# Kernel optimization log

Hardware: AMD Instinct MI355X
Metric: run time of the kernel (lower is better)

Reference implementation:

```python
import jax, jax.numpy as jnp
import numpy as np

B, T, D_MODEL, H, D = 2, 2048, 2048, 16, 128


def _rope_tables(t, d_half, base=10000.0):
    inv_freq = 1.0 / (base ** (jnp.arange(d_half, dtype=jnp.float32) / d_half))
    ang = jnp.arange(t, dtype=jnp.float32)[:, None] * inv_freq[None, :]  # (T, D/2)
    return jnp.cos(ang), jnp.sin(ang)


def setup_inputs() -> dict:
    key = jax.random.key(0)
    ks = jax.random.split(key, 5)
    x = jax.random.normal(ks[0], (B, T, D_MODEL), dtype=jnp.float32)
    mask = jnp.tril(jnp.ones((T, T), dtype=bool))  # causal boolean mask
    cos, sin = _rope_tables(T, D // 2)
    std = 1.0 / np.sqrt(D_MODEL)
    Wq = jax.random.normal(ks[1], (D_MODEL, H * D), dtype=jnp.float32) * std
    Wk = jax.random.normal(ks[2], (D_MODEL, H * D), dtype=jnp.float32) * std
    Wv = jax.random.normal(ks[3], (D_MODEL, H * D), dtype=jnp.float32) * std
    Wo = jax.random.normal(ks[4], (H * D, D_MODEL), dtype=jnp.float32) * std
    return {"x": x, "mask": mask, "cos": cos, "sin": sin,
            "Wq": Wq, "Wk": Wk, "Wv": Wv, "Wo": Wo}


def _apply_rope(x, cos, sin):
    # x: (B, H, T, D); cos/sin: (T, D/2)
    half = x.shape[-1] // 2
    x1, x2 = x[..., :half], x[..., half:]
    c = cos[None, None]
    s = sin[None, None]
    return jnp.concatenate([x1 * c - x2 * s, x1 * s + x2 * c], axis=-1)


def reference(x, mask, cos, sin, Wq, Wk, Wv, Wo):
    b, t, _ = x.shape
    scale = 1.0 / np.sqrt(D)
    # projections: (B, T, H*D) -> (B, H, T, D)
    q = (x @ Wq).reshape(b, t, H, D).transpose(0, 2, 1, 3)
    k = (x @ Wk).reshape(b, t, H, D).transpose(0, 2, 1, 3)
    v = (x @ Wv).reshape(b, t, H, D).transpose(0, 2, 1, 3)
    q = _apply_rope(q, cos, sin)
    k = _apply_rope(k, cos, sin)
    scores = jnp.einsum('bhqd,bhkd->bhqk', q, k) * scale
    scores = jnp.where(mask[None, None], scores, jnp.float32(-1e30))
    attn = jax.nn.softmax(scores, axis=-1)
    out = jnp.einsum('bhqk,bhkd->bhqd', attn, v)  # (B, H, T, D)
    out = out.transpose(0, 2, 1, 3).reshape(b, t, H * D)
    return out @ Wo
```

## Files before the change

kernel.cpp:

```cpp
#include <hip/hip_runtime.h>

#define T_SEQ 2048
#define DM    2048
#define NH    16
#define HD    128
#define NROW  4096

typedef __attribute__((ext_vector_type(8))) short short8;
typedef __attribute__((ext_vector_type(4))) float f32x4;

static __device__ __forceinline__ float bf2f(unsigned short h) {
    unsigned int u = ((unsigned int)h) << 16;
    return __builtin_bit_cast(float, u);
}
static __device__ __forceinline__ unsigned short f2bf(float f) {
    unsigned int u = __builtin_bit_cast(unsigned int, f);
    u += 0x7FFFu + ((u >> 16) & 1u);
    return (unsigned short)(u >> 16);
}
static __device__ __forceinline__ unsigned short bf_fast(float f) {
    return (unsigned short)((__builtin_bit_cast(unsigned int, f) + 0x8000u) >> 16);
}

typedef __attribute__((address_space(1))) const unsigned int gas_uint;
typedef __attribute__((address_space(3))) unsigned int las_uint;

static __device__ __forceinline__ void load_lds16(const void* g, void* l) {
    __builtin_amdgcn_global_load_lds((gas_uint*)g, (las_uint*)l, 16, 0, 0);
}

static __device__ __forceinline__ f32x4 mfma_bf16(short8 a, short8 b, f32x4 c) {
    return __builtin_amdgcn_mfma_f32_16x16x32_bf16(a, b, c, 0, 0, 0);
}

__global__ __launch_bounds__(256) void k_cast(const float* __restrict__ x,
                                              unsigned short* __restrict__ xb, int n) {
    int idx = (blockIdx.x * 256 + threadIdx.x) * 4;
    if (idx >= n) return;
    float4 v = *(const float4*)(x + idx);
    ushort4 o;
    o.x = f2bf(v.x); o.y = f2bf(v.y); o.z = f2bf(v.z); o.w = f2bf(v.w);
    *(ushort4*)(xb + idx) = o;
}

__global__ __launch_bounds__(256) void k_transpose(const float* __restrict__ w0, const float* __restrict__ w1,
                                                   const float* __restrict__ w2, const float* __restrict__ w3,
                                                   unsigned short* __restrict__ t0, unsigned short* __restrict__ t1,
                                                   unsigned short* __restrict__ t2, unsigned short* __restrict__ t3) {
    __shared__ float tile[32][33];
    int z = blockIdx.z;
    const float* W = (z == 0) ? w0 : (z == 1) ? w1 : (z == 2) ? w2 : w3;
    unsigned short* Wt = (z == 0) ? t0 : (z == 1) ? t1 : (z == 2) ? t2 : t3;
    int bx = blockIdx.x * 32;
    int by = blockIdx.y * 32;
    int tx = threadIdx.x, ty = threadIdx.y;
#pragma unroll
    for (int i = 0; i < 4; ++i)
        tile[ty + i * 8][tx] = W[(size_t)(by + ty + i * 8) * DM + bx + tx];
    __syncthreads();
#pragma unroll
    for (int i = 0; i < 4; ++i)
        Wt[(size_t)(bx + ty + i * 8) * DM + by + tx] = f2bf(tile[tx][ty + i * 8]);
}

template <bool FOUT>
static __device__ __forceinline__ void gemm_body(const unsigned short* __restrict__ A,
                                                 const unsigned short* __restrict__ Bt,
                                                 unsigned short* __restrict__ Cb,
                                                 float* __restrict__ Cf) {
    __shared__ unsigned short As[128 * 64];
    __shared__ unsigned short Bs[128 * 64];
    const int tid = threadIdx.x;
    const int w = tid >> 6, lane = tid & 63;
    const int col = lane & 15, quad = lane >> 4;
    const int wm = w >> 1, wn = w & 1;
    const size_t m0 = (size_t)blockIdx.y * 128;
    const size_t n0 = (size_t)blockIdx.x * 128;

    f32x4 acc[4][4];
#pragma unroll
    for (int i = 0; i < 4; ++i)
#pragma unroll
        for (int j = 0; j < 4; ++j)
            acc[i][j] = (f32x4){0.f, 0.f, 0.f, 0.f};

    const int lrow = lane >> 3;
    const int gcol = ((lane & 7) ^ lrow) * 8;

    for (int k0 = 0; k0 < DM; k0 += 64) {
#pragma unroll
        for (int c = w; c < 16; c += 4) {
            load_lds16(A + (m0 + c * 8 + lrow) * DM + k0 + gcol, &As[c * 512]);
            load_lds16(Bt + (n0 + c * 8 + lrow) * DM + k0 + gcol, &Bs[c * 512]);
        }
        __syncthreads();
#pragma unroll
        for (int ks = 0; ks < 2; ++ks) {
            short8 af[4], bf[4];
            int g = ks * 4 + quad;
#pragma unroll
            for (int mt = 0; mt < 4; ++mt) {
                int r = wm * 64 + mt * 16 + col;
                af[mt] = *(const short8*)&As[r * 64 + ((g ^ (r & 7)) * 8)];
            }
#pragma unroll
            for (int nt = 0; nt < 4; ++nt) {
                int r = wn * 64 + nt * 16 + col;
                bf[nt] = *(const short8*)&Bs[r * 64 + ((g ^ (r & 7)) * 8)];
            }
#pragma unroll
            for (int mt = 0; mt < 4; ++mt)
#pragma unroll
                for (int nt = 0; nt < 4; ++nt)
                    acc[mt][nt] = mfma_bf16(af[mt], bf[nt], acc[mt][nt]);
        }
        __syncthreads();
    }
#pragma unroll
    for (int mt = 0; mt < 4; ++mt)
#pragma unroll
        for (int nt = 0; nt < 4; ++nt)
#pragma unroll
            for (int reg = 0; reg < 4; ++reg) {
                size_t r = m0 + wm * 64 + mt * 16 + quad * 4 + reg;
                size_t c = n0 + wn * 64 + nt * 16 + col;
                if (FOUT) Cf[r * DM + c] = acc[mt][nt][reg];
                else      Cb[r * DM + c] = f2bf(acc[mt][nt][reg]);
            }
}

__global__ __launch_bounds__(256) void k_gemm_qkv(const unsigned short* __restrict__ xb,
                                                  const unsigned short* __restrict__ wtq,
                                                  const unsigned short* __restrict__ wtk,
                                                  const unsigned short* __restrict__ wtv,
                                                  unsigned short* __restrict__ qb,
                                                  unsigned short* __restrict__ kb,
                                                  unsigned short* __restrict__ vb) {
    int z = blockIdx.z;
    const unsigned short* Bt = (z == 0) ? wtq : (z == 1) ? wtk : wtv;
    unsigned short* C = (z == 0) ? qb : (z == 1) ? kb : vb;
    gemm_body<false>(xb, Bt, C, nullptr);
}

__global__ __launch_bounds__(256) void k_gemm_out(const unsigned short* __restrict__ ob,
                                                  const unsigned short* __restrict__ wto,
                                                  float* __restrict__ out) {
    gemm_body<true>(ob, wto, nullptr, out);
}

__global__ __launch_bounds__(256) void k_rope_k(unsigned short* __restrict__ K,
                                                const float* __restrict__ cosp,
                                                const float* __restrict__ sinp) {
    int idx = blockIdx.x * 256 + threadIdx.x;
    int d4 = (idx & 15) * 4;
    int h = (idx >> 4) & 15;
    int row = idx >> 8;
    int t = row & (T_SEQ - 1);
    size_t base = (size_t)row * DM + h * HD + d4;
    ushort4 x1 = *(const ushort4*)(K + base);
    ushort4 x2 = *(const ushort4*)(K + base + 64);
    float4 c = *(const float4*)(cosp + t * 64 + d4);
    float4 s = *(const float4*)(sinp + t * 64 + d4);
    ushort4 o1, o2;
#pragma unroll
    for (int i = 0; i < 4; ++i) {
        float a1 = bf2f(((const unsigned short*)&x1)[i]);
        float a2 = bf2f(((const unsigned short*)&x2)[i]);
        float cc = ((const float*)&c)[i], ss = ((const float*)&s)[i];
        ((unsigned short*)&o1)[i] = f2bf(a1 * cc - a2 * ss);
        ((unsigned short*)&o2)[i] = f2bf(a1 * ss + a2 * cc);
    }
    *(ushort4*)(K + base) = o1;
    *(ushort4*)(K + base + 64) = o2;
}

__global__ __launch_bounds__(256) void k_vtr(const unsigned short* __restrict__ V,
                                             unsigned short* __restrict__ Vt) {
    __shared__ unsigned short tile[64][68];
    int t0 = blockIdx.x * 64;
    int hd0 = blockIdx.y * 64;
    int b = blockIdx.z;
    int tid = threadIdx.x;
    int rr = tid >> 4, cc = (tid & 15) * 4;
#pragma unroll
    for (int it = 0; it < 4; ++it) {
        int row = it * 16 + rr;
        *(ushort4*)&tile[row][cc] =
            *(const ushort4*)(V + (size_t)(b * T_SEQ + t0 + row) * DM + hd0 + cc);
    }
    __syncthreads();
    int h = hd0 >> 7, d0 = hd0 & 127;
    size_t obase = (size_t)(b * NH + h) * HD;
#pragma unroll
    for (int it = 0; it < 4; ++it) {
        int lhd = it * 16 + rr;
        ushort4 v;
#pragma unroll
        for (int j = 0; j < 4; ++j) ((unsigned short*)&v)[j] = tile[cc + j][lhd];
        *(ushort4*)(Vt + (obase + d0 + lhd) * (size_t)T_SEQ + t0 + cc) = v;
    }
}

__global__ __launch_bounds__(256) void k_flash(const unsigned short* __restrict__ Q,
                                               const unsigned short* __restrict__ K,
                                               const unsigned short* __restrict__ Vt,
                                               unsigned short* __restrict__ O,
                                               const float* __restrict__ cosp,
                                               const float* __restrict__ sinp) {
    __shared__ unsigned short Ks[64 * 128];
    __shared__ unsigned short Vs[128 * 64];
    __shared__ unsigned short Ps[4 * 16 * 72];
    const int tid = threadIdx.x;
    const int w = tid >> 6, lane = tid & 63;
    const int col = lane & 15, quad = lane >> 4;
    const int h = blockIdx.y, b = blockIdx.z;
    const int txlo = blockIdx.x;
    const int txhi = 31 - txlo;
    const int q0lo = txlo * 64, q0hi = txhi * 64;
    const size_t rowbase = ((size_t)b * T_SEQ) * DM + (size_t)h * HD;
    const size_t hbase = ((size_t)b * NH + h) * HD;
    const float SCL = 0.088388347648318447f * 1.4426950408889634f;

    short8 qlo[4], qhi[4];
    auto load_q = [&](int q0, short8* qf) {
        const int t = q0 + w * 16 + col;
        const unsigned short* qp = Q + rowbase + (size_t)t * DM;
#pragma unroll
        for (int ks = 0; ks < 4; ++ks)
            qf[ks] = *(const short8*)(qp + ks * 32 + quad * 8);
        const float* cp = cosp + t * 64 + quad * 8;
        const float* sp = sinp + t * 64 + quad * 8;
#pragma unroll
        for (int ks = 0; ks < 2; ++ks) {
            float4 c0 = *(const float4*)(cp + ks * 32);
            float4 c1 = *(const float4*)(cp + ks * 32 + 4);
            float4 s0 = *(const float4*)(sp + ks * 32);
            float4 s1 = *(const float4*)(sp + ks * 32 + 4);
#pragma unroll
            for (int j = 0; j < 8; ++j) {
                float cv = ((j < 4) ? ((const float*)&c0)[j] : ((const float*)&c1)[j - 4]) * SCL;
                float sv = ((j < 4) ? ((const float*)&s0)[j] : ((const float*)&s1)[j - 4]) * SCL;
                float a1 = bf2f((unsigned short)qf[ks][j]);
                float a2 = bf2f((unsigned short)qf[ks + 2][j]);
                qf[ks][j]     = (short)f2bf(a1 * cv - a2 * sv);
                qf[ks + 2][j] = (short)f2bf(a1 * sv + a2 * cv);
            }
        }
    };
    load_q(q0lo, qlo);
    load_q(q0hi, qhi);

    f32x4 olo[8], ohi[8];
    float mlo[4], llo[4], mhi[4], lhi[4];
#pragma unroll
    for (int i = 0; i < 8; ++i) {
        olo[i] = (f32x4){0.f, 0.f, 0.f, 0.f};
        ohi[i] = (f32x4){0.f, 0.f, 0.f, 0.f};
    }
#pragma unroll
    for (int r = 0; r < 4; ++r) {
        mlo[r] = -1e30f; llo[r] = 0.f;
        mhi[r] = -1e30f; lhi[r] = 0.f;
    }

    auto tile_step = [&](const short8* qf, f32x4* o, float* m_i, float* l_i,
                         bool diag, int q0t, int k0) {
        f32x4 s[4];
#pragma unroll
        for (int i = 0; i < 4; ++i) s[i] = (f32x4){0.f, 0.f, 0.f, 0.f};
#pragma unroll
        for (int ks = 0; ks < 4; ++ks) {
            const int g = ks * 4 + quad;
#pragma unroll
            for (int nt = 0; nt < 4; ++nt) {
                const int key = nt * 16 + col;
                short8 bfr = *(const short8*)&Ks[key * 128 + ((g ^ (key & 7)) * 8)];
                s[nt] = mfma_bf16(qf[ks], bfr, s[nt]);
            }
        }
        if (diag) {
#pragma unroll
            for (int nt = 0; nt < 4; ++nt)
#pragma unroll
                for (int reg = 0; reg < 4; ++reg)
                    if (k0 + nt * 16 + col > q0t + w * 16 + quad * 4 + reg)
                        s[nt][reg] = -1e30f;
        }
        float alpha[4];
#pragma unroll
        for (int reg = 0; reg < 4; ++reg) {
            float mx = fmaxf(fmaxf(s[0][reg], s[1][reg]), fmaxf(s[2][reg], s[3][reg]));
            mx = fmaxf(mx, __shfl_xor(mx, 1));
            mx = fmaxf(mx, __shfl_xor(mx, 2));
            mx = fmaxf(mx, __shfl_xor(mx, 4));
            mx = fmaxf(mx, __shfl_xor(mx, 8));
            float mnew = fmaxf(m_i[reg], mx);
            alpha[reg] = __builtin_amdgcn_exp2f(m_i[reg] - mnew);
            m_i[reg] = mnew;
            float sum = 0.f;
            const int prow = w * 16 + quad * 4 + reg;
#pragma unroll
            for (int nt = 0; nt < 4; ++nt) {
                float p = __builtin_amdgcn_exp2f(s[nt][reg] - mnew);
                sum += p;
                Ps[prow * 72 + nt * 16 + col] = bf_fast(p);
            }
            sum += __shfl_xor(sum, 1);
            sum += __shfl_xor(sum, 2);
            sum += __shfl_xor(sum, 4);
            sum += __shfl_xor(sum, 8);
            l_i[reg] = l_i[reg] * alpha[reg] + sum;
        }
        f32x4 av = {alpha[0], alpha[1], alpha[2], alpha[3]};
#pragma unroll
        for (int nt2 = 0; nt2 < 8; ++nt2) o[nt2] *= av;
#pragma unroll
        for (int ks2 = 0; ks2 < 2; ++ks2) {
            short8 a = *(const short8*)&Ps[(w * 16 + col) * 72 + ks2 * 32 + quad * 8];
            const int g = ks2 * 4 + quad;
#pragma unroll
            for (int nt2 = 0; nt2 < 8; ++nt2) {
                const int d = nt2 * 16 + col;
                short8 bfr = *(const short8*)&Vs[d * 64 + ((g ^ (d & 7)) * 8)];
                o[nt2] = mfma_bf16(a, bfr, o[nt2]);
            }
        }
    };

    for (int kt = 0; kt <= txhi; ++kt) {
        const int k0 = kt * 64;
        __syncthreads();
#pragma unroll
        for (int c = 0; c < 4; ++c) {
            const int c4 = w * 4 + c;
            const int krow = c4 * 4 + (lane >> 4);
            const int kpos = lane & 15;
            load_lds16(K + rowbase + (size_t)(k0 + krow) * DM + ((kpos ^ (krow & 7)) * 8),
                       &Ks[c4 * 512]);
            const int vrow = c4 * 8 + (lane >> 3);
            const int vpos = lane & 7;
            load_lds16(Vt + (hbase + vrow) * (size_t)T_SEQ + k0 + ((vpos ^ (vrow & 7)) * 8),
                       &Vs[c4 * 512]);
        }
        __syncthreads();
        tile_step(qhi, ohi, mhi, lhi, kt == txhi, q0hi, k0);
        if (kt <= txlo)
            tile_step(qlo, olo, mlo, llo, kt == txlo, q0lo, k0);
    }

    auto finish = [&](const f32x4* o, const float* l_i, int q0t) {
#pragma unroll
        for (int reg = 0; reg < 4; ++reg) {
            float inv = __builtin_amdgcn_rcpf(l_i[reg]);
            unsigned short* op = O + rowbase + (size_t)(q0t + w * 16 + quad * 4 + reg) * DM;
#pragma unroll
            for (int nt2 = 0; nt2 < 8; ++nt2)
                op[nt2 * 16 + col] = bf_fast(o[nt2][reg] * inv);
        }
    };
    finish(olo, llo, q0lo);
    finish(ohi, lhi, q0hi);
}

extern "C" void kernel_launch(void* const* d_in, const int* in_sizes, int n_in,
                              void* d_out, int out_size, void* d_ws, size_t ws_size,
                              hipStream_t stream) {
    const float* x    = (const float*)d_in[0];
    const float* cosp = (const float*)d_in[2];
    const float* sinp = (const float*)d_in[3];
    const float* Wq   = (const float*)d_in[4];
    const float* Wk   = (const float*)d_in[5];
    const float* Wv   = (const float*)d_in[6];
    const float* Wo   = (const float*)d_in[7];
    float* out = (float*)d_out;

    unsigned short* xb  = (unsigned short*)d_ws;
    unsigned short* wtq = xb  + (size_t)NROW * DM;
    unsigned short* wtk = wtq + (size_t)DM * DM;
    unsigned short* wtv = wtk + (size_t)DM * DM;
    unsigned short* wto = wtv + (size_t)DM * DM;
    unsigned short* qb  = wto + (size_t)DM * DM;
    unsigned short* kb  = qb  + (size_t)NROW * DM;
    unsigned short* vb  = kb  + (size_t)NROW * DM;
    unsigned short* ob  = vb  + (size_t)NROW * DM;
    unsigned short* vt  = xb;

    hipLaunchKernelGGL(k_cast, dim3(8192), dim3(256), 0, stream, x, xb, NROW * DM);
    hipLaunchKernelGGL(k_transpose, dim3(64, 64, 4), dim3(32, 8), 0, stream,
                       Wq, Wk, Wv, Wo, wtq, wtk, wtv, wto);
    hipLaunchKernelGGL(k_gemm_qkv, dim3(16, 32, 3), dim3(256), 0, stream,
                       xb, wtq, wtk, wtv, qb, kb, vb);
    hipLaunchKernelGGL(k_rope_k, dim3(4096), dim3(256), 0, stream, kb, cosp, sinp);
    hipLaunchKernelGGL(k_vtr, dim3(32, 32, 2), dim3(256), 0, stream, vb, vt);
    hipLaunchKernelGGL(k_flash, dim3(16, NH, 2), dim3(256), 0, stream,
                       qb, kb, vt, ob, cosp, sinp);
    hipLaunchKernelGGL(k_gemm_out, dim3(16, 32, 1), dim3(256), 0, stream, ob, wto, out);
}
```

Before: 458.9 us.

## Compute transposed S^T and O^T in flash attention to cut softmax shuffles

Swaps the MFMA operand order so each lane owns one query row (S^T = K·Q^T, O^T = V^T·P^T). Row max and sum then need only two cross-quad shuffles instead of four per register, and the per-lane running max/sum drop to scalars. K and V fragments loaded from LDS are shared between the hi and lo query tiles, and P uses separate LDS buffers per tile. P stores and output stores become 4-wide vector writes, at the cost of doubled P scratch and interleaved MFMA issue.

```diff
diff --git a/kernel.cpp b/kernel.cpp
--- a/kernel.cpp
+++ b/kernel.cpp
@@ -201,6 +201,7 @@
     }
 }
 
+#define PSTR 72
 __global__ __launch_bounds__(256) void k_flash(const unsigned short* __restrict__ Q,
                                                const unsigned short* __restrict__ K,
                                                const unsigned short* __restrict__ Vt,
@@ -209,7 +210,7 @@
                                                const float* __restrict__ sinp) {
     __shared__ unsigned short Ks[64 * 128];
     __shared__ unsigned short Vs[128 * 64];
-    __shared__ unsigned short Ps[4 * 16 * 72];
+    __shared__ unsigned short Ps[8][16 * PSTR];
     const int tid = threadIdx.x;
     const int w = tid >> 6, lane = tid & 63;
     const int col = lane & 15, quad = lane >> 4;
@@ -221,6 +222,9 @@
     const size_t hbase = ((size_t)b * NH + h) * HD;
     const float SCL = 0.088388347648318447f * 1.4426950408889634f;
 
+    unsigned short* Ph = &Ps[w][0];
+    unsigned short* Pl = &Ps[w + 4][0];
+
     short8 qlo[4], qhi[4];
     auto load_q = [&](int q0, short8* qf) {
         const int t = q0 + w * 16 + col;
@@ -251,84 +255,58 @@
     load_q(q0hi, qhi);
 
     f32x4 olo[8], ohi[8];
-    float mlo[4], llo[4], mhi[4], lhi[4];
 #pragma unroll
     for (int i = 0; i < 8; ++i) {
         olo[i] = (f32x4){0.f, 0.f, 0.f, 0.f};
         ohi[i] = (f32x4){0.f, 0.f, 0.f, 0.f};
     }
-#pragma unroll
-    for (int r = 0; r < 4; ++r) {
-        mlo[r] = -1e30f; llo[r] = 0.f;
-        mhi[r] = -1e30f; lhi[r] = 0.f;
-    }
-
-    auto tile_step = [&](const short8* qf, f32x4* o, float* m_i, float* l_i,
-                         bool diag, int q0t, int k0) {
-        f32x4 s[4];
-#pragma unroll
-        for (int i = 0; i < 4; ++i) s[i] = (f32x4){0.f, 0.f, 0.f, 0.f};
-#pragma unroll
-        for (int ks = 0; ks < 4; ++ks) {
-            const int g = ks * 4 + quad;
-#pragma unroll
-            for (int nt = 0; nt < 4; ++nt) {
-                const int key = nt * 16 + col;
-                short8 bfr = *(const short8*)&Ks[key * 128 + ((g ^ (key & 7)) * 8)];
-                s[nt] = mfma_bf16(qf[ks], bfr, s[nt]);
-            }
-        }
+    float mlo = -1e30f, llo_s = 0.f, mhi = -1e30f, lhi_s = 0.f;
+
+    auto softmax_st = [&](f32x4* s, f32x4* o, float& m_i, float& l_i,
+                          bool diag, int qg, int k0, unsigned short* P) {
         if (diag) {
 #pragma unroll
-            for (int nt = 0; nt < 4; ++nt)
+            for (int mt = 0; mt < 4; ++mt)
 #pragma unroll
                 for (int reg = 0; reg < 4; ++reg)
-                    if (k0 + nt * 16 + col > q0t + w * 16 + quad * 4 + reg)
-                        s[nt][reg] = -1e30f;
-        }
-        float alpha[4];
-#pragma unroll
-        for (int reg = 0; reg < 4; ++reg) {
-            float mx = fmaxf(fmaxf(s[0][reg], s[1][reg]), fmaxf(s[2][reg], s[3][reg]));
-            mx = fmaxf(mx, __shfl_xor(mx, 1));
-            mx = fmaxf(mx, __shfl_xor(mx, 2));
-            mx = fmaxf(mx, __shfl_xor(mx, 4));
-            mx = fmaxf(mx, __shfl_xor(mx, 8));
-            float mnew = fmaxf(m_i[reg], mx);
-            alpha[reg] = __builtin_amdgcn_exp2f(m_i[reg] - mnew);
-            m_i[reg] = mnew;
-            float sum = 0.f;
-            const int prow = w * 16 + quad * 4 + reg;
-#pragma unroll
-            for (int nt = 0; nt < 4; ++nt) {
-                float p = __builtin_amdgcn_exp2f(s[nt][reg] - mnew);
-                sum += p;
-                Ps[prow * 72 + nt * 16 + col] = bf_fast(p);
-            }
-            sum += __shfl_xor(sum, 1);
-            sum += __shfl_xor(sum, 2);
-            sum += __shfl_xor(sum, 4);
-            sum += __shfl_xor(sum, 8);
-            l_i[reg] = l_i[reg] * alpha[reg] + sum;
-        }
-        f32x4 av = {alpha[0], alpha[1], alpha[2], alpha[3]};
-#pragma unroll
-        for (int nt2 = 0; nt2 < 8; ++nt2) o[nt2] *= av;
-#pragma unroll
-        for (int ks2 = 0; ks2 < 2; ++ks2) {
-            short8 a = *(const short8*)&Ps[(w * 16 + col) * 72 + ks2 * 32 + quad * 8];
-            const int g = ks2 * 4 + quad;
-#pragma unroll
-            for (int nt2 = 0; nt2 < 8; ++nt2) {
-                const int d = nt2 * 16 + col;
-                short8 bfr = *(const short8*)&Vs[d * 64 + ((g ^ (d & 7)) * 8)];
-                o[nt2] = mfma_bf16(a, bfr, o[nt2]);
-            }
-        }
+                    if (k0 + mt * 16 + quad * 4 + reg > qg)
+                        s[mt][reg] = -1e30f;
+        }
+        float mx = -1e30f;
+#pragma unroll
+        for (int mt = 0; mt < 4; ++mt)
+#pragma unroll
+            for (int reg = 0; reg < 4; ++reg) mx = fmaxf(mx, s[mt][reg]);
+        mx = fmaxf(mx, __shfl_xor(mx, 16));
+        mx = fmaxf(mx, __shfl_xor(mx, 32));
+        float mnew = fmaxf(m_i, mx);
+        float alpha = __builtin_amdgcn_exp2f(m_i - mnew);
+        m_i = mnew;
+        float sum = 0.f;
+#pragma unroll
+        for (int mt = 0; mt < 4; ++mt) {
+            float p0 = __builtin_amdgcn_exp2f(s[mt][0] - mnew);
+            float p1 = __builtin_amdgcn_exp2f(s[mt][1] - mnew);
+            float p2 = __builtin_amdgcn_exp2f(s[mt][2] - mnew);
+            float p3 = __builtin_amdgcn_exp2f(s[mt][3] - mnew);
+            sum += (p0 + p1) + (p2 + p3);
+            ushort4 st;
+            ((unsigned short*)&st)[0] = bf_fast(p0);
+            ((unsigned short*)&st)[1] = bf_fast(p1);
+            ((unsigned short*)&st)[2] = bf_fast(p2);
+            ((unsigned short*)&st)[3] = bf_fast(p3);
+            *(ushort4*)(P + col * PSTR + mt * 16 + quad * 4) = st;
+        }
+        sum += __shfl_xor(sum, 16);
+        sum += __shfl_xor(sum, 32);
+        l_i = l_i * alpha + sum;
+#pragma unroll
+        for (int i = 0; i < 8; ++i) o[i] *= alpha;
     };
 
     for (int kt = 0; kt <= txhi; ++kt) {
         const int k0 = kt * 64;
+        const bool lo_act = (kt <= txlo);
         __syncthreads();
 #pragma unroll
         for (int c = 0; c < 4; ++c) {
@@ -343,23 +321,57 @@
                        &Vs[c4 * 512]);
         }
         __syncthreads();
-        tile_step(qhi, ohi, mhi, lhi, kt == txhi, q0hi, k0);
-        if (kt <= txlo)
-            tile_step(qlo, olo, mlo, llo, kt == txlo, q0lo, k0);
-    }
-
-    auto finish = [&](const f32x4* o, const float* l_i, int q0t) {
-#pragma unroll
-        for (int reg = 0; reg < 4; ++reg) {
-            float inv = __builtin_amdgcn_rcpf(l_i[reg]);
-            unsigned short* op = O + rowbase + (size_t)(q0t + w * 16 + quad * 4 + reg) * DM;
-#pragma unroll
-            for (int nt2 = 0; nt2 < 8; ++nt2)
-                op[nt2 * 16 + col] = bf_fast(o[nt2][reg] * inv);
+
+        f32x4 sh[4], sl[4];
+#pragma unroll
+        for (int i = 0; i < 4; ++i) {
+            sh[i] = (f32x4){0.f, 0.f, 0.f, 0.f};
+            sl[i] = (f32x4){0.f, 0.f, 0.f, 0.f};
+        }
+#pragma unroll
+        for (int c = 0; c < 4; ++c) {
+#pragma unroll
+            for (int mt = 0; mt < 4; ++mt) {
+                const int key = mt * 16 + col;
+                short8 kf = *(const short8*)&Ks[key * 128 + (((c * 4 + quad) ^ (key & 7)) * 8)];
+                sh[mt] = mfma_bf16(kf, qhi[c], sh[mt]);
+                if (lo_act) sl[mt] = mfma_bf16(kf, qlo[c], sl[mt]);
+            }
+        }
+
+        softmax_st(sh, ohi, mhi, lhi_s, kt == txhi, q0hi + w * 16 + col, k0, Ph);
+        if (lo_act)
+            softmax_st(sl, olo, mlo, llo_s, kt == txlo, q0lo + w * 16 + col, k0, Pl);
+
+#pragma unroll
+        for (int c2 = 0; c2 < 2; ++c2) {
+            short8 pbh = *(const short8*)(Ph + col * PSTR + c2 * 32 + quad * 8);
+            short8 pbl;
+            if (lo_act) pbl = *(const short8*)(Pl + col * PSTR + c2 * 32 + quad * 8);
+#pragma unroll
+            for (int mt2 = 0; mt2 < 8; ++mt2) {
+                const int d = mt2 * 16 + col;
+                short8 vf = *(const short8*)&Vs[d * 64 + (((c2 * 4 + quad) ^ (d & 7)) * 8)];
+                ohi[mt2] = mfma_bf16(vf, pbh, ohi[mt2]);
+                if (lo_act) olo[mt2] = mfma_bf16(vf, pbl, olo[mt2]);
+            }
+        }
+    }
+
+    auto finish = [&](const f32x4* o, float l_i, int q0t) {
+        float inv = __builtin_amdgcn_rcpf(l_i);
+        unsigned short* op = O + rowbase + (size_t)(q0t + w * 16 + col) * DM + quad * 4;
+#pragma unroll
+        for (int mt2 = 0; mt2 < 8; ++mt2) {
+            ushort4 st;
+#pragma unroll
+            for (int j = 0; j < 4; ++j)
+                ((unsigned short*)&st)[j] = bf_fast(o[mt2][j] * inv);
+            *(ushort4*)(op + mt2 * 16) = st;
         }
     };
-    finish(olo, llo, q0lo);
-    finish(ohi, lhi, q0hi);
+    finish(olo, llo_s, q0lo);
+    finish(ohi, lhi_s, q0hi);
 }
 
 extern "C" void kernel_launch(void* const* d_in, const int* in_sizes, int n_in,
```

Measured after the change: 551.6 us. +20.2%, slower.
